# Kernel optimization log

Measured on AMD Instinct MI355X. Metric: run time of the kernel, lower is better.

## Reference

```python
import jax, jax.numpy as jnp
import numpy as np

N, E, H = 1024, 2048, 32
DIMS = [4, 128, 512, 1028]
NEG_SLOPE_ATT = 0.2   # GATv2 attention LeakyReLU
NEG_SLOPE_ACT = 0.01  # torch.nn.LeakyReLU default


def _lin(key, fan_in, fan_out):
    k1, k2 = jax.random.split(key)
    s = 1.0 / np.sqrt(fan_in)
    return (jax.random.uniform(k1, (fan_in, fan_out), jnp.float32, -s, s),
            jax.random.uniform(k2, (fan_out,), jnp.float32, -s, s))


def setup_inputs() -> dict:
    key = jax.random.key(0)
    ks = jax.random.split(key, 32)
    inp = {
        'x': jax.random.normal(ks[0], (N, 4), jnp.float32),
        'edge_index': jax.random.randint(ks[1], (2, E), 0, N, jnp.int64),
    }
    # GATv2 layers: lin_l/lin_r -> heads*out, att [H, C], bias [C]
    ki = 2
    for i in range(3):
        cin, cout = DIMS[i], DIMS[i + 1]
        wl, bl = _lin(ks[ki], cin, H * cout); ki += 1
        wr, br = _lin(ks[ki], cin, H * cout); ki += 1
        att = jax.random.normal(ks[ki], (H, cout), jnp.float32) * 0.05; ki += 1
        bias = jnp.zeros((cout,), jnp.float32)
        j = i + 1
        inp.update({f'w{j}l': wl, f'b{j}l': bl, f'w{j}r': wr, f'b{j}r': br,
                    f'att{j}': att, f'gb{j}': bias})
    # decoder MLP 1028 -> 512 -> 128 -> 2
    for j, (cin, cout) in enumerate([(1028, 512), (512, 128), (128, 2)], 1):
        w, b = _lin(ks[ki], cin, cout); ki += 1
        inp[f'dw{j}'] = w
        inp[f'db{j}'] = b
    return inp


def _gatv2(x, src, dst, wl, bl, wr, br, att, bias, cout):
    # lin_l on source nodes, lin_r on target nodes (PyG GATv2Conv)
    xl = (x @ wl + bl).reshape(-1, H, cout)   # [N, H, C]
    xr = (x @ wr + br).reshape(-1, H, cout)
    e = jax.nn.leaky_relu(xl[src] + xr[dst], NEG_SLOPE_ATT)  # [Etot, H, C]
    score = jnp.einsum('ehc,hc->eh', e, att)                  # [Etot, H]
    smax = jax.ops.segment_max(score, dst, num_segments=N)
    alpha = jnp.exp(score - smax[dst])
    denom = jax.ops.segment_sum(alpha, dst, num_segments=N)
    alpha = alpha / denom[dst]
    out = jax.ops.segment_sum(alpha[:, :, None] * xl[src], dst, num_segments=N)
    return out.mean(axis=1) + bias  # concat=False: average heads


def reference(x, edge_index,
              w1l, b1l, w1r, b1r, att1, gb1,
              w2l, b2l, w2r, b2r, att2, gb2,
              w3l, b3l, w3r, b3r, att3, gb3,
              dw1, db1, dw2, db2, dw3, db3):
    # add self loops (PyG default)
    loop = jnp.arange(N, dtype=edge_index.dtype)
    src = jnp.concatenate([edge_index[0], loop])
    dst = jnp.concatenate([edge_index[1], loop])

    act = lambda z: jax.nn.leaky_relu(z, NEG_SLOPE_ACT)
    z = _gatv2(x, src, dst, w1l, b1l, w1r, b1r, att1, gb1, 128)
    z = act(z)
    z = _gatv2(z, src, dst, w2l, b2l, w2r, b2r, att2, gb2, 512)
    z = act(z)
    z = _gatv2(z, src, dst, w3l, b3l, w3r, b3r, att3, gb3, 1028)

    z = act(z @ dw1 + db1)
    z = act(z @ dw2 + db2)
    z = z @ dw3 + db3  # [N, 2]
    return z.reshape(-1)
```

## Files before the change

kernel.cpp:

```cpp
#include <hip/hip_runtime.h>
#include <cstdint>
#include <cstddef>

#define NN 1024
#define EE 2048
#define ETOT 3072
#define HH 32

typedef __bf16 bf16_t;
typedef __attribute__((ext_vector_type(8))) __bf16 bf16x8;
typedef __attribute__((ext_vector_type(4))) __bf16 bf16x4;
typedef __attribute__((ext_vector_type(2))) __bf16 bf16x2;
typedef __attribute__((ext_vector_type(4))) float f32x4;

typedef const __attribute__((address_space(1))) void gvoid_t;
typedef __attribute__((address_space(3))) void lvoid_t;

__device__ __forceinline__ void gll16(const void* g, void* l) {
    __builtin_amdgcn_global_load_lds((gvoid_t*)g, (lvoid_t*)l, 16, 0, 0);
}

__global__ void k_zero_int(int* p, int n) {
    int i = blockIdx.x * 256 + threadIdx.x;
    if (i < n) p[i] = 0;
}

__global__ void k_detect(const int* ei, int* flag) {
    int i = blockIdx.x * 256 + threadIdx.x;
    int idx = 2 * i + 1;
    if (idx < 2 * EE && ei[idx] != 0) atomicOr(flag, 1);
}

__global__ void k_edge_prep(const int* ei, const int* flag, int* srcA, int* dstA, int* cnt) {
    int e = blockIdx.x * 256 + threadIdx.x;
    if (e >= ETOT) return;
    int s, d;
    if (e < EE) {
        if (*flag) { s = ei[e]; d = ei[EE + e]; }
        else       { s = ei[2 * e]; d = ei[2 * (EE + e)]; }
        s &= (NN - 1); d &= (NN - 1);
    } else {
        s = d = e - EE;
    }
    srcA[e] = s; dstA[e] = d;
    atomicAdd(&cnt[d], 1);
}

__global__ void k_scan(const int* cnt, int* off) {
    __shared__ int sh[NN];
    int t = threadIdx.x;
    sh[t] = cnt[t];
    __syncthreads();
    for (int o = 1; o < NN; o <<= 1) {
        int v = (t >= o) ? sh[t - o] : 0;
        __syncthreads();
        sh[t] += v;
        __syncthreads();
    }
    off[t + 1] = sh[t];
    if (t == 0) off[0] = 0;
}

__global__ void k_fill(const int* dstA, const int* off, int* cur, int* csre) {
    int e = blockIdx.x * 256 + threadIdx.x;
    if (e >= ETOT) return;
    int d = dstA[e];
    int p = atomicAdd(&cur[d], 1);
    csre[off[d] + p] = e;
}

__global__ void k_convA(const float* __restrict__ A, bf16_t* __restrict__ Ab,
                        int M, int K, int Kp) {
    int idx = blockIdx.x * 256 + threadIdx.x;
    if (idx >= M * Kp) return;
    int m = idx / Kp, k = idx % Kp;
    Ab[idx] = (k < K) ? (bf16_t)A[(size_t)m * K + k] : (bf16_t)0.f;
}

__global__ void k_convB(const float* __restrict__ B, bf16_t* __restrict__ Bt,
                        int K, int Nsub, int ldb, int Kp) {
    __shared__ float sh[32][33];
    int kt = blockIdx.y * 32, nt = blockIdx.x * 32;
    int tx = threadIdx.x & 31, ty = threadIdx.x >> 5;
#pragma unroll
    for (int i = 0; i < 4; ++i) {
        int k = kt + ty + i * 8, n = nt + tx;
        sh[ty + i * 8][tx] = (k < K && n < Nsub) ? B[(size_t)k * ldb + n] : 0.f;
    }
    __syncthreads();
    int kq = (threadIdx.x & 7) * 4;
    int nl = threadIdx.x >> 3;
    int n = nt + nl;
    if (n < Nsub) {
        bf16x4 v;
        v[0] = (bf16_t)sh[kq][nl];
        v[1] = (bf16_t)sh[kq + 1][nl];
        v[2] = (bf16_t)sh[kq + 2][nl];
        v[3] = (bf16_t)sh[kq + 3][nl];
        *(bf16x4*)(&Bt[(size_t)n * Kp + kt + kq]) = v;
    }
}

__global__ __launch_bounds__(256) void k_gemm_bf16(
        const bf16_t* __restrict__ Ab, const bf16_t* __restrict__ Bt,
        const float* __restrict__ bias, void* __restrict__ Cm,
        int M, int Nsub, int Kp, int act, int obf) {
    __shared__ __align__(16) bf16_t SH[32768];
    int tid = threadIdx.x;
    int wave = tid >> 6, lane = tid & 63;
    int wm = (wave & 1) * 64, wn = (wave >> 1) * 64;
    int l16 = lane & 15, lq = lane >> 4;

    int nx = gridDim.x, ny = gridDim.y;
    int bx = blockIdx.x, by = blockIdx.y;
    int total = nx * ny;
    if ((total & 7) == 0) {
        int j = bx + nx * by;
        int w = (j & 7) * (total >> 3) + (j >> 3);
        bx = w / ny;
        by = w % ny;
    }
    int m0 = by * 128, n0 = bx * 128;

    const bf16_t* gA[4];
    const bf16_t* gB[4];
#pragma unroll
    for (int i = 0; i < 4; ++i) {
        int u = wave * 64 + lane + i * 256;
        int r = u >> 3, s = u & 7;
        int c = ((s ^ (r & 7)) << 3);
        gA[i] = Ab + (size_t)(m0 + r) * Kp + c;
        gB[i] = Bt + (size_t)(n0 + r) * Kp + c;
    }

    f32x4 acc[4][4] = {};
    int nt = Kp >> 6;

    {
        bf16_t* dA = SH + wave * 512;
#pragma unroll
        for (int i = 0; i < 4; ++i) {
            gll16(gA[i], dA + i * 2048);
            gll16(gB[i], dA + 8192 + i * 2048);
            gA[i] += 64; gB[i] += 64;
        }
    }
    asm volatile("s_waitcnt vmcnt(0)" ::: "memory");
    asm volatile("s_barrier" ::: "memory");
    __builtin_amdgcn_sched_barrier(0);

    int bc = 0;
    for (int t = 0; t < nt; ++t) {
        if (t + 1 < nt) {
            bf16_t* dA = SH + (bc ^ 1) * 16384 + wave * 512;
#pragma unroll
            for (int i = 0; i < 4; ++i) {
                gll16(gA[i], dA + i * 2048);
                gll16(gB[i], dA + 8192 + i * 2048);
                gA[i] += 64; gB[i] += 64;
            }
        }
        __builtin_amdgcn_sched_barrier(0);
        const bf16_t* rb = SH + bc * 16384;
        bf16x8 af[2][4], bfr[2][4];
#pragma unroll
        for (int kk = 0; kk < 2; ++kk) {
            int cs = (((kk * 4 + lq) ^ (l16 & 7)) << 3);
#pragma unroll
            for (int mi = 0; mi < 4; ++mi)
                af[kk][mi] = *(const bf16x8*)(rb + (wm + mi * 16 + l16) * 64 + cs);
#pragma unroll
            for (int ni = 0; ni < 4; ++ni)
                bfr[kk][ni] = *(const bf16x8*)(rb + 8192 + (wn + ni * 16 + l16) * 64 + cs);
        }
#pragma unroll
        for (int kk = 0; kk < 2; ++kk)
#pragma unroll
            for (int mi = 0; mi < 4; ++mi)
#pragma unroll
                for (int ni = 0; ni < 4; ++ni)
                    acc[mi][ni] = __builtin_amdgcn_mfma_f32_16x16x32_bf16(
                        af[kk][mi], bfr[kk][ni], acc[mi][ni], 0, 0, 0);
        asm volatile("s_waitcnt vmcnt(0) lgkmcnt(0)" ::: "memory");
        asm volatile("s_barrier" ::: "memory");
        __builtin_amdgcn_sched_barrier(0);
        bc ^= 1;
    }

    if (obf) {
#pragma unroll
        for (int ni = 0; ni < 4; ++ni) {
            int cl = wn + ni * 16 + l16;
            float bv = bias[n0 + cl];
#pragma unroll
            for (int mi = 0; mi < 4; ++mi)
#pragma unroll
                for (int r = 0; r < 4; ++r) {
                    int rl = wm + mi * 16 + lq * 4 + r;
                    float v = acc[mi][ni][r] + bv;
                    if (act && v < 0.f) v *= 0.01f;
                    int slot = ((cl >> 3) ^ (rl & 7)) & 15;
                    SH[rl * 128 + slot * 8 + (cl & 7)] = (bf16_t)v;
                }
        }
        __syncthreads();
        bf16_t* Cb = (bf16_t*)Cm;
#pragma unroll
        for (int i = 0; i < 8; ++i) {
            int j = i * 2048 + tid * 8;
            int rl = j >> 7;
            int p = (j >> 3) & 15;
            int cl = ((p ^ (rl & 7)) & 15) * 8;
            bf16x8 v = *(const bf16x8*)(SH + rl * 128 + p * 8);
            int row = m0 + rl, col = n0 + cl;
            if (row < M) {
                if (col + 7 < Nsub) {
                    *(bf16x8*)(Cb + (size_t)row * Nsub + col) = v;
                } else {
#pragma unroll
                    for (int e = 0; e < 8; ++e)
                        if (col + e < Nsub) Cb[(size_t)row * Nsub + col + e] = v[e];
                }
            }
        }
    } else {
#pragma unroll
        for (int ni = 0; ni < 4; ++ni) {
            int col = n0 + wn + ni * 16 + l16;
            if (col >= Nsub) continue;
            float bv = bias[col];
#pragma unroll
            for (int mi = 0; mi < 4; ++mi)
#pragma unroll
                for (int r = 0; r < 4; ++r) {
                    int row = m0 + wm + mi * 16 + lq * 4 + r;
                    if (row < M) {
                        float v = acc[mi][ni][r] + bv;
                        if (act && v < 0.f) v *= 0.01f;
                        ((float*)Cm)[(size_t)row * Nsub + col] = v;
                    }
                }
        }
    }
}

#define TM 64
#define TN 64
#define TK 16
__global__ __launch_bounds__(256) void k_gemm(
        const float* __restrict__ A, const float* __restrict__ B,
        const float* __restrict__ bias, void* __restrict__ Cm,
        int M, int Nsub, int K, int ldb, int act, int obf) {
    __shared__ float As[TK][TM];
    __shared__ float Bs[TK][TN];
    int tid = threadIdx.x;
    int tx = tid % 16, ty = tid / 16;
    int m0 = blockIdx.y * TM, n0 = blockIdx.x * TN;
    float acc[4][4] = {};
    for (int k0 = 0; k0 < K; k0 += TK) {
#pragma unroll
        for (int i = 0; i < 4; ++i) {
            int idx = tid * 4 + i;
            int m = idx >> 4, k = idx & 15;
            float v = 0.f;
            if (k0 + k < K && m0 + m < M) v = A[(size_t)(m0 + m) * K + k0 + k];
            As[k][m] = v;
        }
#pragma unroll
        for (int i = 0; i < 4; ++i) {
            int idx = tid * 4 + i;
            int k = idx >> 6, n = idx & 63;
            float v = 0.f;
            if (k0 + k < K && n0 + n < Nsub) v = B[(size_t)(k0 + k) * ldb + n0 + n];
            Bs[k][n] = v;
        }
        __syncthreads();
#pragma unroll
        for (int kk = 0; kk < TK; ++kk) {
            float4 a4 = *(const float4*)&As[kk][ty * 4];
            float4 b4 = *(const float4*)&Bs[kk][tx * 4];
            float af[4] = {a4.x, a4.y, a4.z, a4.w};
            float bf[4] = {b4.x, b4.y, b4.z, b4.w};
#pragma unroll
            for (int i = 0; i < 4; ++i)
#pragma unroll
                for (int j = 0; j < 4; ++j)
                    acc[i][j] += af[i] * bf[j];
        }
        __syncthreads();
    }
#pragma unroll
    for (int i = 0; i < 4; ++i) {
        int m = m0 + ty * 4 + i;
        if (m >= M) continue;
#pragma unroll
        for (int j = 0; j < 4; ++j) {
            int n = n0 + tx * 4 + j;
            if (n < Nsub) {
                float v = acc[i][j] + bias[n];
                if (act && v < 0.f) v *= 0.01f;
                if (obf) ((bf16_t*)Cm)[(size_t)m * Nsub + n] = (bf16_t)v;
                else     ((float*)Cm)[(size_t)m * Nsub + n] = v;
            }
        }
    }
}

__global__ void k_gemm_naive(const float* __restrict__ A, const float* __restrict__ B,
                             const float* __restrict__ bias, float* __restrict__ out,
                             int M, int N, int K, int act) {
    int idx = blockIdx.x * 256 + threadIdx.x;
    if (idx >= M * N) return;
    int m = idx / N, n = idx % N;
    float s = bias[n];
    for (int k = 0; k < K; ++k)
        s += A[(size_t)m * K + k] * B[(size_t)k * N + n];
    if (act && s < 0.f) s *= 0.01f;
    out[idx] = s;
}

__global__ void k_score(const bf16_t* __restrict__ xl, const bf16_t* __restrict__ xr,
                        const float* __restrict__ att, const int* __restrict__ srcA,
                        const int* __restrict__ dstA, float* __restrict__ sc,
                        int C, int HG, int h0) {
    int wid = (blockIdx.x * 256 + threadIdx.x) >> 6;
    int lane = threadIdx.x & 63;
    if (wid >= ETOT * HG) return;
    int e = wid / HG, hl = wid % HG;
    int s = srcA[e], d = dstA[e];
    const bf16x4* pl = (const bf16x4*)(xl + ((size_t)s * HG + hl) * C);
    const bf16x4* pr = (const bf16x4*)(xr + ((size_t)d * HG + hl) * C);
    const float4* pa = (const float4*)(att + (size_t)(h0 + hl) * C);
    float acc = 0.f;
    int C4 = C >> 2;
    for (int c = lane; c < C4; c += 64) {
        bf16x4 a = pl[c], b = pr[c];
        float4 w = pa[c];
        float v;
        v = (float)a[0] + (float)b[0]; v = v > 0.f ? v : 0.2f * v; acc += v * w.x;
        v = (float)a[1] + (float)b[1]; v = v > 0.f ? v : 0.2f * v; acc += v * w.y;
        v = (float)a[2] + (float)b[2]; v = v > 0.f ? v : 0.2f * v; acc += v * w.z;
        v = (float)a[3] + (float)b[3]; v = v > 0.f ? v : 0.2f * v; acc += v * w.w;
    }
#pragma unroll
    for (int off = 32; off; off >>= 1) acc += __shfl_down(acc, off, 64);
    if (lane == 0) sc[(size_t)e * HH + h0 + hl] = acc;
}

__global__ void k_softmax(const int* __restrict__ off, const int* __restrict__ csre,
                          float* __restrict__ sc, int HG, int h0) {
    int idx = blockIdx.x * 256 + threadIdx.x;
    if (idx >= NN * HG) return;
    int d = idx / HG, h = h0 + idx % HG;
    int b = off[d], en = off[d + 1];
    float m = -1e30f;
    for (int i = b; i < en; ++i) m = fmaxf(m, sc[(size_t)csre[i] * HH + h]);
    float ssum = 0.f;
    for (int i = b; i < en; ++i) ssum += expf(sc[(size_t)csre[i] * HH + h] - m);
    float inv = 1.f / ssum;
    for (int i = b; i < en; ++i) {
        size_t p = (size_t)csre[i] * HH + h;
        sc[p] = expf(sc[p] - m) * inv;
    }
}

__global__ __launch_bounds__(256) void k_aggregate(
        const bf16_t* __restrict__ xl, const float* __restrict__ sc,
        const int* __restrict__ off, const int* __restrict__ csre,
        const int* __restrict__ srcA, const float* __restrict__ bias,
        float* __restrict__ z, int C, int HG, int h0, int lgNC,
        int first, int last, int act) {
    __shared__ float4 sh[256];
    int d = blockIdx.x;
    int NC = 1 << lgNC;
    int c4i = threadIdx.x & (NC - 1);
    int hl = threadIdx.x >> lgNC;
    int c4 = blockIdx.y * NC + c4i;
    int C4 = C >> 2;
    bool active = (c4 < C4);
    float4 acc = {0.f, 0.f, 0.f, 0.f};
    int b = off[d], en = off[d + 1];
    for (int i = b; i < en; ++i) {
        int e = csre[i];
        int s = srcA[e];
        float w = sc[(size_t)e * HH + h0 + hl];
        if (active) {
            bf16x4 vx = *((const bf16x4*)(xl + ((size_t)s * HG + hl) * C) + c4);
            acc.x += w * (float)vx[0];
            acc.y += w * (float)vx[1];
            acc.z += w * (float)vx[2];
            acc.w += w * (float)vx[3];
        }
    }
    sh[threadIdx.x] = acc;
    __syncthreads();
    for (int s = HG >> 1; s >= 1; s >>= 1) {
        if (hl < s) {
            float4 o = sh[threadIdx.x + (s << lgNC)];
            float4 m = sh[threadIdx.x];
            m.x += o.x; m.y += o.y; m.z += o.z; m.w += o.w;
            sh[threadIdx.x] = m;
        }
        __syncthreads();
    }
    if (hl == 0 && active) {
        acc = sh[threadIdx.x];
        float4* zp = (float4*)(z + (size_t)d * C) + c4;
        if (!first) {
            float4 prev = *zp;
            acc.x += prev.x; acc.y += prev.y; acc.z += prev.z; acc.w += prev.w;
        }
        if (last) {
            const float4 bz = *((const float4*)bias + c4);
            acc.x = acc.x * (1.f / 32.f) + bz.x;
            acc.y = acc.y * (1.f / 32.f) + bz.y;
            acc.z = acc.z * (1.f / 32.f) + bz.z;
            acc.w = acc.w * (1.f / 32.f) + bz.w;
            if (act) {
                acc.x = acc.x < 0.f ? acc.x * 0.01f : acc.x;
                acc.y = acc.y < 0.f ? acc.y * 0.01f : acc.y;
                acc.z = acc.z < 0.f ? acc.z * 0.01f : acc.z;
                acc.w = acc.w < 0.f ? acc.w * 0.01f : acc.w;
            }
        }
        *zp = acc;
    }
}

extern "C" void kernel_launch(void* const* d_in, const int* in_sizes, int n_in,
                              void* d_out, int out_size, void* d_ws, size_t ws_size,
                              hipStream_t stream) {
    const float* x   = (const float*)d_in[0];
    const int* ei    = (const int*)d_in[1];
    const float* w1l = (const float*)d_in[2];  const float* b1l = (const float*)d_in[3];
    const float* w1r = (const float*)d_in[4];  const float* b1r = (const float*)d_in[5];
    const float* att1= (const float*)d_in[6];  const float* gb1 = (const float*)d_in[7];
    const float* w2l = (const float*)d_in[8];  const float* b2l = (const float*)d_in[9];
    const float* w2r = (const float*)d_in[10]; const float* b2r = (const float*)d_in[11];
    const float* att2= (const float*)d_in[12]; const float* gb2 = (const float*)d_in[13];
    const float* w3l = (const float*)d_in[14]; const float* b3l = (const float*)d_in[15];
    const float* w3r = (const float*)d_in[16]; const float* b3r = (const float*)d_in[17];
    const float* att3= (const float*)d_in[18]; const float* gb3 = (const float*)d_in[19];
    const float* dw1 = (const float*)d_in[20]; const float* db1 = (const float*)d_in[21];
    const float* dw2 = (const float*)d_in[22]; const float* db2 = (const float*)d_in[23];
    const float* dw3 = (const float*)d_in[24]; const float* db3 = (const float*)d_in[25];
    float* outp = (float*)d_out;

    char* p = (char*)d_ws;
    auto alloc = [&](size_t bytes) -> char* {
        char* r = p;
        p += (bytes + 255) & ~(size_t)255;
        return r;
    };
    float* sc   = (float*)alloc((size_t)ETOT * HH * 4);
    float* za   = (float*)alloc((size_t)NN * 1028 * 4);
    float* zb   = (float*)alloc((size_t)NN * 1028 * 4);
    bf16_t* Abf = (bf16_t*)alloc((size_t)NN * 1088 * 2);
    int*   ints = (int*)  alloc((size_t)(2 * NN + 16) * 4);
    int* cnt  = ints;
    int* cur  = ints + NN;
    int* flag = ints + 2 * NN;
    int* offp = (int*)alloc((size_t)(NN + 1) * 4);
    int* csre = (int*)alloc((size_t)ETOT * 4);
    int* srcA = (int*)alloc((size_t)ETOT * 4);
    int* dstA = (int*)alloc((size_t)ETOT * 4);
    size_t used = (size_t)(p - (char*)d_ws);
    size_t remain = (ws_size > used) ? (ws_size - used) : 0;
    char* chunk = p;

    k_zero_int<<<dim3((2 * NN + 16 + 255) / 256), dim3(256), 0, stream>>>(ints, 2 * NN + 16);
    k_detect<<<dim3((EE + 255) / 256), dim3(256), 0, stream>>>(ei, flag);
    k_edge_prep<<<dim3((ETOT + 255) / 256), dim3(256), 0, stream>>>(ei, flag, srcA, dstA, cnt);
    k_scan<<<dim3(1), dim3(NN), 0, stream>>>(cnt, offp);
    k_fill<<<dim3((ETOT + 255) / 256), dim3(256), 0, stream>>>(dstA, offp, cur, csre);

    struct Layer {
        const float* in; int cin; int C;
        const float *wl, *bl, *wr, *br, *att, *gb;
        float* zout; int act;
    };
    Layer L[3] = {
        { x,    4, 128,  w1l, b1l, w1r, b1r, att1, gb1, za, 1 },
        { za, 128, 512,  w2l, b2l, w2r, b2r, att2, gb2, zb, 1 },
        { zb, 512, 1028, w3l, b3l, w3r, b3r, att3, gb3, za, 0 },
    };
    auto al = [](size_t n) { return (n + 127) & ~(size_t)127; };

    for (int li = 0; li < 3; ++li) {
        int C = L[li].C, K = L[li].cin;
        bool mfma = (K >= 128);
        int Kp = (K + 63) & ~63;
        size_t perHG = 2ull * NN * C * 2 + (mfma ? (size_t)C * Kp * 2 : 0);
        int HG = 32;
        while (HG > 1 && (size_t)HG * perHG + (1u << 20) > remain) HG >>= 1;
        int nchunk = HH / HG;
        int lgNC = 0;
        while ((1 << lgNC) * HG < 256) ++lgNC;
        int NC = 1 << lgNC;
        bf16_t* xlc = (bf16_t*)chunk;
        bf16_t* xrc = xlc + al((size_t)NN * HG * C);
        bf16_t* Bt  = xrc + al((size_t)NN * HG * C);

        if (mfma)
            k_convA<<<dim3((NN * Kp + 255) / 256), dim3(256), 0, stream>>>(L[li].in, Abf, NN, K, Kp);

        for (int hg = 0; hg < nchunk; ++hg) {
            int h0 = hg * HG;
            int colOff = h0 * C;
            int Nsub = HG * C;
            if (mfma) {
                dim3 gc((Nsub + 31) / 32, Kp / 32);
                dim3 gg((Nsub + 127) / 128, NN / 128);
                k_convB<<<gc, dim3(256), 0, stream>>>(L[li].wl + colOff, Bt, K, Nsub, HH * C, Kp);
                k_gemm_bf16<<<gg, dim3(256), 0, stream>>>(Abf, Bt, L[li].bl + colOff, xlc, NN, Nsub, Kp, 0, 1);
                k_convB<<<gc, dim3(256), 0, stream>>>(L[li].wr + colOff, Bt, K, Nsub, HH * C, Kp);
                k_gemm_bf16<<<gg, dim3(256), 0, stream>>>(Abf, Bt, L[li].br + colOff, xrc, NN, Nsub, Kp, 0, 1);
            } else {
                dim3 gg((Nsub + TN - 1) / TN, (NN + TM - 1) / TM);
                k_gemm<<<gg, dim3(256), 0, stream>>>(L[li].in, L[li].wl + colOff, L[li].bl + colOff,
                                                     xlc, NN, Nsub, K, HH * C, 0, 1);
                k_gemm<<<gg, dim3(256), 0, stream>>>(L[li].in, L[li].wr + colOff, L[li].br + colOff,
                                                     xrc, NN, Nsub, K, HH * C, 0, 1);
            }
            int waves = ETOT * HG;
            k_score<<<dim3((waves * 64 + 255) / 256), dim3(256), 0, stream>>>(
                xlc, xrc, L[li].att, srcA, dstA, sc, C, HG, h0);
            k_softmax<<<dim3((NN * HG + 255) / 256), dim3(256), 0, stream>>>(offp, csre, sc, HG, h0);
            int C4 = C >> 2;
            dim3 ga(NN, (C4 + NC - 1) / NC);
            k_aggregate<<<ga, dim3(256), 0, stream>>>(xlc, sc, offp, csre, srcA, L[li].gb,
                                                      L[li].zout, C, HG, h0, lgNC,
                                                      hg == 0, hg == nchunk - 1, L[li].act);
        }
    }

    {
        bf16_t* Bt1  = (bf16_t*)chunk;
        bf16_t* AbD2 = Bt1 + al((size_t)512 * 1088);
        bf16_t* Bt2  = AbD2 + al((size_t)NN * 512);

        k_convA<<<dim3((NN * 1088 + 255) / 256), dim3(256), 0, stream>>>(za, Abf, NN, 1028, 1088);
        k_convB<<<dim3(512 / 32, 1088 / 32), dim3(256), 0, stream>>>(dw1, Bt1, 1028, 512, 512, 1088);
        k_gemm_bf16<<<dim3(512 / 128, NN / 128), dim3(256), 0, stream>>>(Abf, Bt1, db1, AbD2, NN, 512, 1088, 1, 1);

        k_convB<<<dim3(128 / 32, 512 / 32), dim3(256), 0, stream>>>(dw2, Bt2, 512, 128, 128, 512);
        k_gemm_bf16<<<dim3(128 / 128, NN / 128), dim3(256), 0, stream>>>(AbD2, Bt2, db2, za, NN, 128, 512, 1, 0);
    }
    k_gemm_naive<<<dim3((NN * 2 + 255) / 256), dim3(256), 0, stream>>>(za, dw3, db3, outp, NN, 2, 128, 0);
}
```

Measured before the change: 678.2 us.

## Fuse lin_l and lin_r GEMMs into one dual-output MFMA kernel sharing A tiles

Adds a dual GEMM kernel that loads each A tile once and multiplies it against both the lin_l and lin_r weight tiles, writing both outputs. This replaces two separate GEMM launches per head group and halves the reads of A. The B buffers are now held separately, which doubles the workspace reserved for them and may shrink the head-group size. The kernel uses triple-buffered LDS with twice the accumulators, which raises register pressure. Separately, the score kernel now maps waves edge-major within each head, which changes its memory access pattern.

```diff
diff --git a/kernel.cpp b/kernel.cpp
--- a/kernel.cpp
+++ b/kernel.cpp
@@ -99,6 +99,138 @@
         v[3] = (bf16_t)sh[kq + 3][nl];
         *(bf16x4*)(&Bt[(size_t)n * Kp + kt + kq]) = v;
     }
+}
+
+#define DBUFE 12288
+__global__ __launch_bounds__(256, 2) void k_gemm_bf16_dual(
+        const bf16_t* __restrict__ Ab, const bf16_t* __restrict__ Btl,
+        const bf16_t* __restrict__ Btr,
+        const float* __restrict__ biasl, const float* __restrict__ biasr,
+        bf16_t* __restrict__ Cl, bf16_t* __restrict__ Cr,
+        int M, int Nsub, int Kp) {
+    __shared__ __align__(16) bf16_t SH[36864];
+    int tid = threadIdx.x;
+    int wave = tid >> 6, lane = tid & 63;
+    int wm = (wave & 1) * 64, wn = (wave >> 1) * 64;
+    int l16 = lane & 15, lq = lane >> 4;
+
+    int nx = gridDim.x, ny = gridDim.y;
+    int bx = blockIdx.x, by = blockIdx.y;
+    int total = nx * ny;
+    if ((total & 7) == 0) {
+        int j = bx + nx * by;
+        int w = (j & 7) * (total >> 3) + (j >> 3);
+        bx = w / ny;
+        by = w % ny;
+    }
+    int m0 = by * 128, n0 = bx * 128;
+
+    int u0 = wave * 128 + lane;
+    int u1 = u0 + 64;
+    int r0 = u0 >> 2, s0 = u0 & 3;
+    int r1 = u1 >> 2, s1 = u1 & 3;
+    int c0 = ((s0 ^ ((r0 >> 1) & 3)) << 3);
+    int c1 = ((s1 ^ ((r1 >> 1) & 3)) << 3);
+    const bf16_t* gA0 = Ab  + (size_t)(m0 + r0) * Kp + c0;
+    const bf16_t* gA1 = Ab  + (size_t)(m0 + r1) * Kp + c1;
+    const bf16_t* gL0 = Btl + (size_t)(n0 + r0) * Kp + c0;
+    const bf16_t* gL1 = Btl + (size_t)(n0 + r1) * Kp + c1;
+    const bf16_t* gR0 = Btr + (size_t)(n0 + r0) * Kp + c0;
+    const bf16_t* gR1 = Btr + (size_t)(n0 + r1) * Kp + c1;
+
+    int cR = ((lq ^ ((l16 >> 1) & 3)) << 3);
+
+    f32x4 accl[4][4] = {};
+    f32x4 accr[4][4] = {};
+    int nt = Kp >> 5;
+
+#pragma unroll
+    for (int pt = 0; pt < 2; ++pt) {
+        bf16_t* d = SH + pt * DBUFE + wave * 1024;
+        gll16(gA0, d);        gll16(gA1, d + 512);
+        gll16(gL0, d + 4096); gll16(gL1, d + 4096 + 512);
+        gll16(gR0, d + 8192); gll16(gR1, d + 8192 + 512);
+        gA0 += 32; gA1 += 32; gL0 += 32; gL1 += 32; gR0 += 32; gR1 += 32;
+    }
+
+    int bc = 0, bn = 2;
+    for (int t = 0; t < nt; ++t) {
+        if (t + 1 < nt)
+            asm volatile("s_waitcnt vmcnt(6) lgkmcnt(0)" ::: "memory");
+        else
+            asm volatile("s_waitcnt vmcnt(0) lgkmcnt(0)" ::: "memory");
+        asm volatile("s_barrier" ::: "memory");
+        __builtin_amdgcn_sched_barrier(0);
+        if (t + 2 < nt) {
+            bf16_t* d = SH + bn * DBUFE + wave * 1024;
+            gll16(gA0, d);        gll16(gA1, d + 512);
+            gll16(gL0, d + 4096); gll16(gL1, d + 4096 + 512);
+            gll16(gR0, d + 8192); gll16(gR1, d + 8192 + 512);
+            gA0 += 32; gA1 += 32; gL0 += 32; gL1 += 32; gR0 += 32; gR1 += 32;
+        }
+        const bf16_t* rb = SH + bc * DBUFE;
+        bf16x8 af[4], bfl[4], bfr[4];
+#pragma unroll
+        for (int mi = 0; mi < 4; ++mi)
+            af[mi] = *(const bf16x8*)(rb + (wm + mi * 16 + l16) * 32 + cR);
+#pragma unroll
+        for (int ni = 0; ni < 4; ++ni) {
+            bfl[ni] = *(const bf16x8*)(rb + 4096 + (wn + ni * 16 + l16) * 32 + cR);
+            bfr[ni] = *(const bf16x8*)(rb + 8192 + (wn + ni * 16 + l16) * 32 + cR);
+        }
+#pragma unroll
+        for (int mi = 0; mi < 4; ++mi)
+#pragma unroll
+            for (int ni = 0; ni < 4; ++ni) {
+                accl[mi][ni] = __builtin_amdgcn_mfma_f32_16x16x32_bf16(
+                    af[mi], bfl[ni], accl[mi][ni], 0, 0, 0);
+                accr[mi][ni] = __builtin_amdgcn_mfma_f32_16x16x32_bf16(
+                    af[mi], bfr[ni], accr[mi][ni], 0, 0, 0);
+            }
+        bc = (bc == 2) ? 0 : bc + 1;
+        bn = (bn == 2) ? 0 : bn + 1;
+    }
+    asm volatile("s_waitcnt lgkmcnt(0)" ::: "memory");
+    asm volatile("s_barrier" ::: "memory");
+    __builtin_amdgcn_sched_barrier(0);
+
+#define EPILOGUE(ACC, BIAS, CP)                                               \
+    {                                                                         \
+        _Pragma("unroll")                                                     \
+        for (int ni = 0; ni < 4; ++ni) {                                      \
+            int cl = wn + ni * 16 + l16;                                      \
+            float bv = BIAS[n0 + cl];                                         \
+            _Pragma("unroll")                                                 \
+            for (int mi = 0; mi < 4; ++mi)                                    \
+                _Pragma("unroll")                                             \
+                for (int r = 0; r < 4; ++r) {                                 \
+                    int rl = wm + mi * 16 + lq * 4 + r;                       \
+                    float v = ACC[mi][ni][r] + bv;                            \
+                    int slot = ((cl >> 3) ^ (rl & 7)) & 15;                   \
+                    SH[rl * 128 + slot * 8 + (cl & 7)] = (bf16_t)v;           \
+                }                                                             \
+        }                                                                     \
+        __syncthreads();                                                      \
+        _Pragma("unroll")                                                     \
+        for (int i = 0; i < 8; ++i) {                                         \
+            int j = i * 2048 + tid * 8;                                       \
+            int rl = j >> 7;                                                  \
+            int p = (j >> 3) & 15;                                            \
+            int cl = ((p ^ (rl & 7)) & 15) * 8;                               \
+            bf16x8 v = *(const bf16x8*)(SH + rl * 128 + p * 8);               \
+            int row = m0 + rl, col = n0 + cl;                                 \
+            if (row < M && col + 7 < Nsub)                                    \
+                *(bf16x8*)(CP + (size_t)row * Nsub + col) = v;                \
+            else if (row < M)                                                 \
+                for (int e = 0; e < 8; ++e)                                   \
+                    if (col + e < Nsub) CP[(size_t)row * Nsub + col + e] = v[e]; \
+        }                                                                     \
+    }
+
+    EPILOGUE(accl, biasl, Cl)
+    __syncthreads();
+    EPILOGUE(accr, biasr, Cr)
+#undef EPILOGUE
 }
 
 __global__ __launch_bounds__(256) void k_gemm_bf16(
@@ -326,7 +458,7 @@
     int wid = (blockIdx.x * 256 + threadIdx.x) >> 6;
     int lane = threadIdx.x & 63;
     if (wid >= ETOT * HG) return;
-    int e = wid / HG, hl = wid % HG;
+    int e = wid % ETOT, hl = wid / ETOT;
     int s = srcA[e], d = dstA[e];
     const bf16x4* pl = (const bf16x4*)(xl + ((size_t)s * HG + hl) * C);
     const bf16x4* pr = (const bf16x4*)(xr + ((size_t)d * HG + hl) * C);
@@ -490,7 +622,7 @@
         int C = L[li].C, K = L[li].cin;
         bool mfma = (K >= 128);
         int Kp = (K + 63) & ~63;
-        size_t perHG = 2ull * NN * C * 2 + (mfma ? (size_t)C * Kp * 2 : 0);
+        size_t perHG = 2ull * NN * C * 2 + (mfma ? 2ull * C * Kp * 2 : 0);
         int HG = 32;
         while (HG > 1 && (size_t)HG * perHG + (1u << 20) > remain) HG >>= 1;
         int nchunk = HH / HG;
@@ -499,7 +631,8 @@
         int NC = 1 << lgNC;
         bf16_t* xlc = (bf16_t*)chunk;
         bf16_t* xrc = xlc + al((size_t)NN * HG * C);
-        bf16_t* Bt  = xrc + al((size_t)NN * HG * C);
+        bf16_t* Btl = xrc + al((size_t)NN * HG * C);
+        bf16_t* Btr = Btl + al((size_t)HG * C * Kp);
 
         if (mfma)
             k_convA<<<dim3((NN * Kp + 255) / 256), dim3(256), 0, stream>>>(L[li].in, Abf, NN, K, Kp);
@@ -511,10 +644,11 @@
             if (mfma) {
                 dim3 gc((Nsub + 31) / 32, Kp / 32);
                 dim3 gg((Nsub + 127) / 128, NN / 128);
-                k_convB<<<gc, dim3(256), 0, stream>>>(L[li].wl + colOff, Bt, K, Nsub, HH * C, Kp);
-                k_gemm_bf16<<<gg, dim3(256), 0, stream>>>(Abf, Bt, L[li].bl + colOff, xlc, NN, Nsub, Kp, 0, 1);
-                k_convB<<<gc, dim3(256), 0, stream>>>(L[li].wr + colOff, Bt, K, Nsub, HH * C, Kp);
-                k_gemm_bf16<<<gg, dim3(256), 0, stream>>>(Abf, Bt, L[li].br + colOff, xrc, NN, Nsub, Kp, 0, 1);
+                k_convB<<<gc, dim3(256), 0, stream>>>(L[li].wl + colOff, Btl, K, Nsub, HH * C, Kp);
+                k_convB<<<gc, dim3(256), 0, stream>>>(L[li].wr + colOff, Btr, K, Nsub, HH * C, Kp);
+                k_gemm_bf16_dual<<<gg, dim3(256), 0, stream>>>(
+                    Abf, Btl, Btr, L[li].bl + colOff, L[li].br + colOff,
+                    xlc, xrc, NN, Nsub, Kp);
             } else {
                 dim3 gg((Nsub + TN - 1) / TN, (NN + TM - 1) / TM);
                 k_gemm<<<gg, dim3(256), 0, stream>>>(L[li].in, L[li].wl + colOff, L[li].bl + colOff,
```

New measurement: 702.4 us. +3.6%, slower.
